# Kernel tuning notes

Measured on AMD Instinct MI355X. Metric: run time of the kernel, lower is better.

Reference implementation:

```python
import jax, jax.numpy as jnp
import numpy as np

N_QUBITS = 16
N_LAYERS = 6
BATCH = 512


def _apply_1q(state, U, q, n, batched):
    """Apply a single-qubit gate U to qubit q of state (B, 2**n).
    U: (2,2) shared, or (B,2,2) per-sample if batched."""
    B = state.shape[0]
    d0, d1 = 2 ** q, 2 ** (n - q - 1)
    s = state.reshape(B, d0, 2, d1)
    if batched:
        s = jnp.einsum('bij,bxjy->bxiy', U, s)
    else:
        s = jnp.einsum('ij,bxjy->bxiy', U, s)
    return s.reshape(B, -1)


def _apply_cnot(state, c, t, n):
    """CNOT with control c, target t on state (B, 2**n)."""
    B = state.shape[0]
    a, b = (c, t) if c < t else (t, c)
    d0, d1, d2 = 2 ** a, 2 ** (b - a - 1), 2 ** (n - b - 1)
    s = state.reshape(B, d0, 2, d1, 2, d2)
    if c < t:  # control = axis 2, target = axis 4: flip target where control==1
        s = jnp.concatenate([s[:, :, :1], jnp.flip(s[:, :, 1:], axis=4)], axis=2)
    else:      # control = axis 4, target = axis 2
        s = jnp.concatenate([s[:, :, :, :, :1], jnp.flip(s[:, :, :, :, 1:], axis=2)], axis=4)
    return s.reshape(B, -1)


def _rx(theta):
    """RX(theta) for a batch of angles -> (B,2,2) complex64."""
    c = jnp.cos(theta * 0.5).astype(jnp.complex64)
    s = (-1j * jnp.sin(theta * 0.5)).astype(jnp.complex64)
    return jnp.stack([jnp.stack([c, s], -1), jnp.stack([s, c], -1)], -2)


def _rot(phi, theta, omega):
    """PennyLane Rot(phi,theta,omega) = RZ(omega) RY(theta) RZ(phi) -> (2,2) complex64."""
    c = jnp.cos(theta * 0.5)
    s = jnp.sin(theta * 0.5)
    m00 = jnp.exp(-0.5j * (phi + omega)) * c
    m01 = -jnp.exp(0.5j * (phi - omega)) * s
    m10 = jnp.exp(-0.5j * (phi - omega)) * s
    m11 = jnp.exp(0.5j * (phi + omega)) * c
    return jnp.stack([jnp.stack([m00, m01]), jnp.stack([m10, m11])]).astype(jnp.complex64)


def _circuit(x, weights, n, n_layers):
    B = x.shape[0]
    state = jnp.zeros((B, 2 ** n), dtype=jnp.complex64).at[:, 0].set(1.0)
    # AngleEmbedding: default rotation is RX(x_q) on wire q (per-sample angles)
    for q in range(n):
        state = _apply_1q(state, _rx(x[:, q]), q, n, batched=True)
    # StronglyEntanglingLayers: Rot on each wire, then ring of CNOTs with range r
    for l in range(n_layers):
        for q in range(n):
            U = _rot(weights[l, q, 0], weights[l, q, 1], weights[l, q, 2])
            state = _apply_1q(state, U, q, n, batched=False)
        r = (l % (n - 1)) + 1  # PennyLane default ranges
        for q in range(n):
            state = _apply_cnot(state, q, (q + r) % n, n)
    # <Z_q> = P(bit_q = 0) - P(bit_q = 1)
    probs = state.real ** 2 + state.imag ** 2  # (B, 2**n)
    exps = []
    for q in range(n):
        p = probs.reshape(B, 2 ** q, 2, -1).sum(axis=(1, 3))  # (B, 2)
        exps.append(p[:, 0] - p[:, 1])
    return jnp.stack(exps, axis=-1)  # (B, n)


def setup_inputs() -> dict:
    key = jax.random.key(0)
    kx, kw = jax.random.split(key)
    x = jax.random.normal(kx, (BATCH, N_QUBITS), dtype=jnp.float32)
    weights = jax.random.normal(kw, (N_LAYERS, N_QUBITS, 3), dtype=jnp.float32)
    return {"x": x, "weights": weights}


def reference(x, weights):
    return _circuit(x, weights, N_QUBITS, N_LAYERS)
```

## Files before the change

### kernel.cpp

```cpp
#include <hip/hip_runtime.h>


#define NTH 512
typedef float v16f __attribute__((ext_vector_type(16)));

template <int I> struct IC { static constexpr int value = I; };
template <int N, int I = 0, typename F>
__device__ __forceinline__ void static_for(F&& f) {
  if constexpr (I < N) { f(IC<I>{}); static_for<N, I + 1>(f); }
}

template <int SH, int E> struct EIdx { static constexpr int v = (E & 1) | ((E >> 1) << SH); };


template <int LB>
__device__ __forceinline__ void rot_local(v16f& ar, v16f& ai, const float* __restrict__ u) {
  const float u00r = u[0], u00i = u[1], u01r = u[2], u01i = u[3];
  const float u10r = u[4], u10i = u[5], u11r = u[6], u11i = u[7];
  static_for<8>([&](auto hc) {
    constexpr int h = hc.value;
    constexpr int e0 = ((h >> LB) << (LB + 1)) | (h & ((1 << LB) - 1));
    constexpr int e1 = e0 | (1 << LB);
    const float axr = ar[e0], axi = ai[e0], bxr = ar[e1], bxi = ai[e1];
    ar[e0] = u00r * axr - u00i * axi + u01r * bxr - u01i * bxi;
    ai[e0] = u00r * axi + u00i * axr + u01r * bxi + u01i * bxr;
    ar[e1] = u10r * axr - u10i * axi + u11r * bxr - u11i * bxi;
    ai[e1] = u10r * axi + u10i * axr + u11r * bxi + u11i * bxr;
  });
}

__device__ __forceinline__ void rot_lane(v16f& ar, v16f& ai, const float* __restrict__ u,
                                         const int m, const int bit) {
  const float car = bit ? u[6] : u[0], cai = bit ? u[7] : u[1];
  const float cbr = bit ? u[4] : u[2], cbi = bit ? u[5] : u[3];
  static_for<16>([&](auto ec) {
    constexpr int e = ec.value;
    const float orr = ar[e], oii = ai[e];
    const float pr = __shfl_xor(orr, m);
    const float pi = __shfl_xor(oii, m);
    ar[e] = car * orr - cai * oii + cbr * pr - cbi * pi;
    ai[e] = car * oii + cai * orr + cbr * pi + cbi * pr;
  });
}

template <int SH, int C>
__device__ __forceinline__ void cnot_lane(v16f& ar, v16f& ai, const int m, const int ibase) {
  if constexpr ((EIdx<SH, 15>::v >> C) & 1) {
    static_for<16>([&](auto ec) {
      constexpr int e = ec.value;
      if constexpr ((EIdx<SH, e>::v >> C) & 1) {
        ar[e] = __shfl_xor(ar[e], m);
        ai[e] = __shfl_xor(ai[e], m);
      }
    });
  } else {
    if ((ibase >> C) & 1) {
      static_for<16>([&](auto ec) {
        constexpr int e = ec.value;
        ar[e] = __shfl_xor(ar[e], m);
        ai[e] = __shfl_xor(ai[e], m);
      });
    }
  }
}

template <int TB, int SH, int C>
__device__ __forceinline__ void cnot_local(v16f& ar, v16f& ai, const int ibase) {
  static_for<8>([&](auto hc) {
    constexpr int h = hc.value;
    constexpr int e0 = ((h >> TB) << (TB + 1)) | (h & ((1 << TB) - 1));
    constexpr int e1 = e0 | (1 << TB);
    if constexpr ((EIdx<SH, 15>::v >> C) & 1) {
      if constexpr ((EIdx<SH, e0>::v >> C) & 1) {
        const float tr = ar[e0], ti = ai[e0];
        ar[e0] = ar[e1]; ai[e0] = ai[e1];
        ar[e1] = tr;     ai[e1] = ti;
      }
    } else {
      const int take = (ibase >> C) & 1;
      const float axr = ar[e0], axi = ai[e0], bxr = ar[e1], bxi = ai[e1];
      ar[e0] = take ? bxr : axr; ai[e0] = take ? bxi : axi;
      ar[e1] = take ? axr : bxr; ai[e1] = take ? axi : bxi;
    }
  });
}

__global__ void qsim_prep(const float* __restrict__ w, float* __restrict__ gm) {
  const int i = threadIdx.x;
  if (i < 96) {
    const float phi = w[i * 3 + 0];
    const float th  = w[i * 3 + 1];
    const float om  = w[i * 3 + 2];
    float st, ct; sincosf(0.5f * th, &st, &ct);
    float sa, ca; sincosf(0.5f * (phi + om), &sa, &ca);
    float sb, cb; sincosf(0.5f * (phi - om), &sb, &cb);
    float* u = gm + i * 8;
    u[0] =  ct * ca; u[1] = -ct * sa;
    u[2] = -st * cb; u[3] = -st * sb;
    u[4] =  st * cb; u[5] = -st * sb;
    u[6] =  ct * ca; u[7] =  ct * sa;
  }
}

template <int L>
__global__ void __launch_bounds__(NTH) sweepP(float2* __restrict__ st,
                                              const float* __restrict__ x,
                                              const float* __restrict__ gm) {
  const int tid = threadIdx.x;
  const int s  = blockIdx.x >> 3;
  const int fb = blockIdx.x & 7;
  const int ibase = (fb << 13) | ((tid & 63) << 4) | ((tid >> 6) << 1);
  const int pbase = (fb << 13) | ((tid & 63) << 1) | ((tid >> 6) << 7);
  float2* __restrict__ base = st + (s << 16) + pbase;
  constexpr int r = L + 1;
  const float* __restrict__ gl = gm + L * 128;
  v16f ar, ai;

  if constexpr (L == 0) {
    __shared__ float iv[16][4];
    if (tid < 16) {
      const float* u = gm + tid * 8;
      float sx, cx; sincosf(0.5f * x[s * 16 + tid], &sx, &cx);
      iv[tid][0] = u[0] * cx + u[3] * sx;
      iv[tid][1] = u[1] * cx - u[2] * sx;
      iv[tid][2] = u[4] * cx + u[7] * sx;
      iv[tid][3] = u[5] * cx - u[6] * sx;
    }
    __syncthreads();
    float Tr = 1.f, Ti = 0.f;
    #pragma unroll
    for (int b = 4; b <= 9; ++b) {
      const int bit = (ibase >> b) & 1;
      const float fr = iv[b][2 * bit], fi = iv[b][2 * bit + 1];
      const float nr = Tr * fr - Ti * fi; Ti = Tr * fi + Ti * fr; Tr = nr;
    }
    #pragma unroll
    for (int b = 13; b <= 15; ++b) {
      const int bit = (ibase >> b) & 1;
      const float fr = iv[b][2 * bit], fi = iv[b][2 * bit + 1];
      const float nr = Tr * fr - Ti * fi; Ti = Tr * fi + Ti * fr; Tr = nr;
    }
    const int b1 = (ibase >> 1) & 1, b2 = (ibase >> 2) & 1, b3 = (ibase >> 3) & 1;
    float Wr[2], Wi[2];
    #pragma unroll
    for (int b0 = 0; b0 < 2; ++b0) {
      const int c1 = b0 ^ b1, c2 = b1 ^ b2, c3 = b2 ^ b3;
      float wr = iv[0][2 * b0], wi = iv[0][2 * b0 + 1];
      { const float fr = iv[1][2 * c1], fi = iv[1][2 * c1 + 1];
        const float nr = wr * fr - wi * fi; wi = wr * fi + wi * fr; wr = nr; }
      { const float fr = iv[2][2 * c2], fi = iv[2][2 * c2 + 1];
        const float nr = wr * fr - wi * fi; wi = wr * fi + wi * fr; wr = nr; }
      { const float fr = iv[3][2 * c3], fi = iv[3][2 * c3 + 1];
        const float nr = wr * fr - wi * fi; wi = wr * fi + wi * fr; wr = nr; }
      Wr[b0] = wr * Tr - wi * Ti; Wi[b0] = wr * Ti + wi * Tr;
    }
    ar[0] = Wr[0]; ai[0] = Wi[0]; ar[1] = Wr[1]; ai[1] = Wi[1];
    static_for<3>([&](auto bc) {
      constexpr int bI = bc.value;
      const int q = 10 + bI;
      const float v0r = iv[q][0], v0i = iv[q][1], v1r = iv[q][2], v1i = iv[q][3];
      static_for<(1 << (bI + 1))>([&](auto kc) {
        constexpr int k = kc.value;
        constexpr int k1 = k | (1 << (bI + 1));
        const float kr = ar[k], ki = ai[k];
        ar[k1] = kr * v1r - ki * v1i; ai[k1] = kr * v1i + ki * v1r;
        ar[k]  = kr * v0r - ki * v0i; ai[k]  = kr * v0i + ki * v0r;
      });
    });
  } else {
    #pragma unroll
    for (int eh = 0; eh < 8; ++eh) {
      const float4 v = *reinterpret_cast<const float4*>(base + (eh << 10));
      ar[2 * eh] = v.x; ai[2 * eh] = v.y; ar[2 * eh + 1] = v.z; ai[2 * eh + 1] = v.w;
    }
    #pragma unroll
    for (int q = 4; q <= 9; ++q)
      rot_lane(ar, ai, gl + q * 8, 1 << (q - 4), (tid >> (q - 4)) & 1);
    rot_local<1>(ar, ai, gl + 80);
    rot_local<2>(ar, ai, gl + 88);
    rot_local<3>(ar, ai, gl + 96);
  }

  constexpr int gstart = (L == 0) ? 3 : (L == 1) ? 2 : (L == 2) ? 1 : 0;
  static_for<(11 - L) - gstart + 1>([&](auto gc) {
    constexpr int g = gstart + gc.value;
    constexpr int t = g + r;
    if constexpr (t <= 9) cnot_lane<10, g>(ar, ai, 1 << (t - 4), ibase);
    else                  cnot_local<t - 9, 10, g>(ar, ai, ibase);
  });

  #pragma unroll
  for (int eh = 0; eh < 8; ++eh)
    *reinterpret_cast<float4*>(base + (eh << 10)) =
        make_float4(ar[2 * eh], ai[2 * eh], ar[2 * eh + 1], ai[2 * eh + 1]);
}

template <int L>
__global__ void __launch_bounds__(NTH) sweepQ(float2* __restrict__ st,
                                              const float* __restrict__ gm,
                                              float* __restrict__ part) {
  const int tid = threadIdx.x;
  const int s  = blockIdx.x >> 3;
  const int fb = blockIdx.x & 7;
  const int ibase = ((tid & 7) << 4) | (((tid >> 3) & 7) << 13) |
                    (((tid >> 6) & 7) << 10) | (fb << 7);
  const int pbase = ((tid & 7) << 1) | (fb << 4) |
                    (((tid >> 6) & 7) << 10) | (((tid >> 3) & 7) << 13);
  float2* __restrict__ base = st + (s << 16) + pbase;
  constexpr int r = L + 1;
  const float* __restrict__ gl = gm + L * 128;
  v16f ar, ai;
  #pragma unroll
  for (int eh = 0; eh < 8; ++eh) {
    const float4 v = *reinterpret_cast<const float4*>(base + (eh << 7));
    ar[2 * eh] = v.x; ai[2 * eh] = v.y; ar[2 * eh + 1] = v.z; ai[2 * eh + 1] = v.w;
  }
  if constexpr (L > 0) {
    rot_lane(ar, ai, gl + 104, 8,  (tid >> 3) & 1);
    rot_lane(ar, ai, gl + 112, 16, (tid >> 4) & 1);
    rot_lane(ar, ai, gl + 120, 32, (tid >> 5) & 1);
  }
  static_for<L + 4>([&](auto gc) {
    constexpr int g = 12 - L + gc.value;
    constexpr int t = (g + r) & 15;
    if constexpr (t >= 13)     cnot_lane<1, g>(ar, ai, 1 << (t - 10), ibase);
    else if constexpr (t >= 4) cnot_lane<1, g>(ar, ai, 1 << (t - 4), ibase);
    else                       cnot_local<t, 1, g>(ar, ai, ibase);
  });

  if constexpr (L < 5) {
    const float* __restrict__ gn = gm + (L + 1) * 128;
    rot_local<0>(ar, ai, gn);
    rot_local<1>(ar, ai, gn + 8);
    rot_local<2>(ar, ai, gn + 16);
    rot_local<3>(ar, ai, gn + 24);
    if constexpr (L == 0) {
      cnot_local<2, 1, 0>(ar, ai, ibase);
      cnot_local<3, 1, 1>(ar, ai, ibase);
    }
    if constexpr (L == 1) {
      cnot_local<3, 1, 0>(ar, ai, ibase);
    }
    #pragma unroll
    for (int eh = 0; eh < 8; ++eh)
      *reinterpret_cast<float4*>(base + (eh << 7)) =
          make_float4(ar[2 * eh], ai[2 * eh], ar[2 * eh + 1], ai[2 * eh + 1]);
  } else {
    __shared__ float red[8][16];
    float tot = 0.f, sl0 = 0.f, sl1 = 0.f, sl2 = 0.f, sl3 = 0.f;
    static_for<16>([&](auto ec) {
      constexpr int e = ec.value;
      const float p = ar[e] * ar[e] + ai[e] * ai[e];
      tot += p;
      if constexpr (e & 1) sl0 -= p; else sl0 += p;
      if constexpr (e & 2) sl1 -= p; else sl1 += p;
      if constexpr (e & 4) sl2 -= p; else sl2 += p;
      if constexpr (e & 8) sl3 -= p; else sl3 += p;
    });
    const float sl[4] = {sl0, sl1, sl2, sl3};
    const int wv = tid >> 6;
    static_for<16>([&](auto qc) {
      constexpr int q = qc.value;
      float v;
      if constexpr (q < 4) v = sl[q];
      else v = ((ibase >> q) & 1) ? -tot : tot;
      v += __shfl_xor(v, 1);  v += __shfl_xor(v, 2);  v += __shfl_xor(v, 4);
      v += __shfl_xor(v, 8);  v += __shfl_xor(v, 16); v += __shfl_xor(v, 32);
      if ((tid & 63) == 0) red[wv][q] = v;
    });
    __syncthreads();
    if (tid < 16) {
      float a = 0.f;
      #pragma unroll
      for (int w8 = 0; w8 < 8; ++w8) a += red[w8][tid];
      part[blockIdx.x * 16 + tid] = a;
    }
  }
}

__global__ void __launch_bounds__(NTH) reduceK(const float* __restrict__ part,
                                               float* __restrict__ out) {
  const int j = blockIdx.x * NTH + threadIdx.x;
  const int s = j >> 4, q = j & 15;
  float a = 0.f;
  #pragma unroll
  for (int fb = 0; fb < 8; ++fb) a += part[(s << 7) + fb * 16 + q];
  out[j] = a;
}

extern "C" void kernel_launch(void* const* d_in, const int* in_sizes, int n_in,
                              void* d_out, int out_size, void* d_ws, size_t ws_size,
                              hipStream_t stream) {
  (void)in_sizes; (void)n_in; (void)out_size;
  const float* x = (const float*)d_in[0];
  const float* w = (const float*)d_in[1];
  float* out = (float*)d_out;
  float* gm   = (float*)d_ws;
  float* part = (float*)((char*)d_ws + 4096);
  float2* st  = (float2*)((char*)d_ws + 524288);

  const size_t avail = ws_size > 524288 ? ws_size - 524288 : 0;
  long long chunk = (long long)(avail / 524288);
  if (chunk > 256) chunk = 256;
  if (chunk < 1) chunk = 1;

  qsim_prep<<<dim3(1), dim3(128), 0, stream>>>(w, gm);
  for (int s0 = 0; s0 < 512; s0 += (int)chunk) {
    const int ns = (512 - s0) < (int)chunk ? (512 - s0) : (int)chunk;
    const dim3 g(ns * 8), b(NTH);
    const float* xs = x + s0 * 16;
    float* pp = part + (size_t)s0 * 128;
    sweepP<0><<<g, b, 0, stream>>>(st, xs, gm);
    sweepQ<0><<<g, b, 0, stream>>>(st, gm, pp);
    sweepP<1><<<g, b, 0, stream>>>(st, xs, gm);
    sweepQ<1><<<g, b, 0, stream>>>(st, gm, pp);
    sweepP<2><<<g, b, 0, stream>>>(st, xs, gm);
    sweepQ<2><<<g, b, 0, stream>>>(st, gm, pp);
    sweepP<3><<<g, b, 0, stream>>>(st, xs, gm);
    sweepQ<3><<<g, b, 0, stream>>>(st, gm, pp);
    sweepP<4><<<g, b, 0, stream>>>(st, xs, gm);
    sweepQ<4><<<g, b, 0, stream>>>(st, gm, pp);
    sweepP<5><<<g, b, 0, stream>>>(st, xs, gm);
    sweepQ<5><<<g, b, 0, stream>>>(st, gm, pp);
  }
  reduceK<<<dim3(16), dim3(NTH), 0, stream>>>(part, out);
}
```

Measured before the change: 1.620 ms.

## Restructure state-vector sweeps with new qubit-to-register mapping and separate final reduction

Changes how qubits map onto register slots, lanes and blocks in both sweep kernels, and moves gates between the P and Q sweeps so the CNOT wrap-around runs at the start of the next P sweep. The final measurement moves into a separate finalK kernel. The aim is to reshape the memory access pattern and gate grouping, for example contiguous float4 loads in sweepP. It adds a thirteenth full pass over the state per chunk, which costs extra global memory traffic.

New measurement: 1.579 ms. -2.5%, faster.

```diff
diff --git a/kernel.cpp b/kernel.cpp
--- a/kernel.cpp
+++ b/kernel.cpp
@@ -109,8 +109,10 @@
   const int tid = threadIdx.x;
   const int s  = blockIdx.x >> 3;
   const int fb = blockIdx.x & 7;
-  const int ibase = (fb << 13) | ((tid & 63) << 4) | ((tid >> 6) << 1);
-  const int pbase = (fb << 13) | ((tid & 63) << 1) | ((tid >> 6) << 7);
+  const int ibase = ((tid & 7) << 4) | (((tid >> 3) & 7) << 7) |
+                    (((tid >> 6) & 7) << 10) | (fb << 13);
+  const int pbase = ((tid & 7) << 1) | (((tid >> 6) & 7) << 7) | (fb << 10) |
+                    (((tid >> 3) & 7) << 13);
   float2* __restrict__ base = st + (s << 16) + pbase;
   constexpr int r = L + 1;
   const float* __restrict__ gl = gm + L * 128;
@@ -129,39 +131,18 @@
     __syncthreads();
     float Tr = 1.f, Ti = 0.f;
     #pragma unroll
-    for (int b = 4; b <= 9; ++b) {
+    for (int b = 4; b <= 15; ++b) {
       const int bit = (ibase >> b) & 1;
       const float fr = iv[b][2 * bit], fi = iv[b][2 * bit + 1];
       const float nr = Tr * fr - Ti * fi; Ti = Tr * fi + Ti * fr; Tr = nr;
     }
-    #pragma unroll
-    for (int b = 13; b <= 15; ++b) {
-      const int bit = (ibase >> b) & 1;
-      const float fr = iv[b][2 * bit], fi = iv[b][2 * bit + 1];
-      const float nr = Tr * fr - Ti * fi; Ti = Tr * fi + Ti * fr; Tr = nr;
-    }
-    const int b1 = (ibase >> 1) & 1, b2 = (ibase >> 2) & 1, b3 = (ibase >> 3) & 1;
-    float Wr[2], Wi[2];
-    #pragma unroll
-    for (int b0 = 0; b0 < 2; ++b0) {
-      const int c1 = b0 ^ b1, c2 = b1 ^ b2, c3 = b2 ^ b3;
-      float wr = iv[0][2 * b0], wi = iv[0][2 * b0 + 1];
-      { const float fr = iv[1][2 * c1], fi = iv[1][2 * c1 + 1];
-        const float nr = wr * fr - wi * fi; wi = wr * fi + wi * fr; wr = nr; }
-      { const float fr = iv[2][2 * c2], fi = iv[2][2 * c2 + 1];
-        const float nr = wr * fr - wi * fi; wi = wr * fi + wi * fr; wr = nr; }
-      { const float fr = iv[3][2 * c3], fi = iv[3][2 * c3 + 1];
-        const float nr = wr * fr - wi * fi; wi = wr * fi + wi * fr; wr = nr; }
-      Wr[b0] = wr * Tr - wi * Ti; Wi[b0] = wr * Ti + wi * Tr;
-    }
-    ar[0] = Wr[0]; ai[0] = Wi[0]; ar[1] = Wr[1]; ai[1] = Wi[1];
-    static_for<3>([&](auto bc) {
+    ar[0] = Tr; ai[0] = Ti;
+    static_for<4>([&](auto bc) {
       constexpr int bI = bc.value;
-      const int q = 10 + bI;
-      const float v0r = iv[q][0], v0i = iv[q][1], v1r = iv[q][2], v1i = iv[q][3];
-      static_for<(1 << (bI + 1))>([&](auto kc) {
+      const float v0r = iv[bI][0], v0i = iv[bI][1], v1r = iv[bI][2], v1i = iv[bI][3];
+      static_for<(1 << bI)>([&](auto kc) {
         constexpr int k = kc.value;
-        constexpr int k1 = k | (1 << (bI + 1));
+        constexpr int k1 = k | (1 << bI);
         const float kr = ar[k], ki = ai[k];
         ar[k1] = kr * v1r - ki * v1i; ai[k1] = kr * v1i + ki * v1r;
         ar[k]  = kr * v0r - ki * v0i; ai[k]  = kr * v0i + ki * v0r;
@@ -170,111 +151,127 @@
   } else {
     #pragma unroll
     for (int eh = 0; eh < 8; ++eh) {
-      const float4 v = *reinterpret_cast<const float4*>(base + (eh << 10));
+      const float4 v = *reinterpret_cast<const float4*>(base + (eh << 4));
       ar[2 * eh] = v.x; ai[2 * eh] = v.y; ar[2 * eh + 1] = v.z; ai[2 * eh + 1] = v.w;
     }
+    static_for<L>([&](auto kc) {
+      constexpr int k = kc.value;
+      constexpr int C = 16 - L + k;
+      if constexpr (k <= 3) cnot_local<k, 1, C>(ar, ai, ibase);
+      else                  cnot_lane<1, C>(ar, ai, 1 << (k - 4), ibase);
+    });
+    rot_local<0>(ar, ai, gl);
+    rot_local<1>(ar, ai, gl + 8);
+    rot_local<2>(ar, ai, gl + 16);
+    rot_local<3>(ar, ai, gl + 24);
     #pragma unroll
     for (int q = 4; q <= 9; ++q)
       rot_lane(ar, ai, gl + q * 8, 1 << (q - 4), (tid >> (q - 4)) & 1);
+  }
+
+  static_for<10 - r>([&](auto gc) {
+    constexpr int g = gc.value;
+    constexpr int t = g + r;
+    if constexpr (t <= 3) cnot_local<t, 1, g>(ar, ai, ibase);
+    else                  cnot_lane<1, g>(ar, ai, 1 << (t - 4), ibase);
+  });
+
+  #pragma unroll
+  for (int eh = 0; eh < 8; ++eh)
+    *reinterpret_cast<float4*>(base + (eh << 4)) =
+        make_float4(ar[2 * eh], ai[2 * eh], ar[2 * eh + 1], ai[2 * eh + 1]);
+}
+
+template <int L>
+__global__ void __launch_bounds__(NTH) sweepQ(float2* __restrict__ st,
+                                              const float* __restrict__ gm) {
+  const int tid = threadIdx.x;
+  const int s  = blockIdx.x >> 3;
+  const int fb = blockIdx.x & 7;
+  const int ibase = ((tid & 7) << 4) | (((tid >> 3) & 7) << 13) |
+                    (((tid >> 6) & 7) << 7) | (fb << 1);
+  const int pbase = ((tid & 7) << 1) | (((tid >> 3) & 7) << 10) |
+                    (((tid >> 6) & 7) << 13) | (fb << 4);
+  float2* __restrict__ base = st + (s << 16) + pbase;
+  constexpr int r = L + 1;
+  const float* __restrict__ gl = gm + L * 128;
+  v16f ar, ai;
+  #pragma unroll
+  for (int eh = 0; eh < 8; ++eh) {
+    const float4 v = *reinterpret_cast<const float4*>(base + (eh << 7));
+    ar[2 * eh] = v.x; ai[2 * eh] = v.y; ar[2 * eh + 1] = v.z; ai[2 * eh + 1] = v.w;
+  }
+  if constexpr (L > 0) {
     rot_local<1>(ar, ai, gl + 80);
     rot_local<2>(ar, ai, gl + 88);
     rot_local<3>(ar, ai, gl + 96);
-  }
-
-  constexpr int gstart = (L == 0) ? 3 : (L == 1) ? 2 : (L == 2) ? 1 : 0;
-  static_for<(11 - L) - gstart + 1>([&](auto gc) {
-    constexpr int g = gstart + gc.value;
+    rot_lane(ar, ai, gl + 104, 8,  (tid >> 3) & 1);
+    rot_lane(ar, ai, gl + 112, 16, (tid >> 4) & 1);
+    rot_lane(ar, ai, gl + 120, 32, (tid >> 5) & 1);
+  }
+  static_for<6>([&](auto gc) {
+    constexpr int g = 10 - r + gc.value;
     constexpr int t = g + r;
-    if constexpr (t <= 9) cnot_lane<10, g>(ar, ai, 1 << (t - 4), ibase);
-    else                  cnot_local<t - 9, 10, g>(ar, ai, ibase);
+    if constexpr (t >= 13) cnot_lane<10, g>(ar, ai, 1 << (t - 10), ibase);
+    else                   cnot_local<t - 9, 10, g>(ar, ai, ibase);
   });
 
   #pragma unroll
   for (int eh = 0; eh < 8; ++eh)
-    *reinterpret_cast<float4*>(base + (eh << 10)) =
+    *reinterpret_cast<float4*>(base + (eh << 7)) =
         make_float4(ar[2 * eh], ai[2 * eh], ar[2 * eh + 1], ai[2 * eh + 1]);
 }
 
-template <int L>
-__global__ void __launch_bounds__(NTH) sweepQ(float2* __restrict__ st,
-                                              const float* __restrict__ gm,
+__global__ void __launch_bounds__(NTH) finalK(const float2* __restrict__ st,
                                               float* __restrict__ part) {
   const int tid = threadIdx.x;
   const int s  = blockIdx.x >> 3;
   const int fb = blockIdx.x & 7;
-  const int ibase = ((tid & 7) << 4) | (((tid >> 3) & 7) << 13) |
-                    (((tid >> 6) & 7) << 10) | (fb << 7);
-  const int pbase = ((tid & 7) << 1) | (fb << 4) |
-                    (((tid >> 6) & 7) << 10) | (((tid >> 3) & 7) << 13);
-  float2* __restrict__ base = st + (s << 16) + pbase;
-  constexpr int r = L + 1;
-  const float* __restrict__ gl = gm + L * 128;
+  const int ibase = ((tid & 7) << 4) | (((tid >> 3) & 7) << 7) |
+                    (((tid >> 6) & 7) << 10) | (fb << 13);
+  const int pbase = ((tid & 7) << 1) | (((tid >> 6) & 7) << 7) | (fb << 10) |
+                    (((tid >> 3) & 7) << 13);
+  const float2* __restrict__ base = st + (s << 16) + pbase;
   v16f ar, ai;
   #pragma unroll
   for (int eh = 0; eh < 8; ++eh) {
-    const float4 v = *reinterpret_cast<const float4*>(base + (eh << 7));
+    const float4 v = *reinterpret_cast<const float4*>(base + (eh << 4));
     ar[2 * eh] = v.x; ai[2 * eh] = v.y; ar[2 * eh + 1] = v.z; ai[2 * eh + 1] = v.w;
   }
-  if constexpr (L > 0) {
-    rot_lane(ar, ai, gl + 104, 8,  (tid >> 3) & 1);
-    rot_lane(ar, ai, gl + 112, 16, (tid >> 4) & 1);
-    rot_lane(ar, ai, gl + 120, 32, (tid >> 5) & 1);
-  }
-  static_for<L + 4>([&](auto gc) {
-    constexpr int g = 12 - L + gc.value;
-    constexpr int t = (g + r) & 15;
-    if constexpr (t >= 13)     cnot_lane<1, g>(ar, ai, 1 << (t - 10), ibase);
-    else if constexpr (t >= 4) cnot_lane<1, g>(ar, ai, 1 << (t - 4), ibase);
-    else                       cnot_local<t, 1, g>(ar, ai, ibase);
-  });
-
-  if constexpr (L < 5) {
-    const float* __restrict__ gn = gm + (L + 1) * 128;
-    rot_local<0>(ar, ai, gn);
-    rot_local<1>(ar, ai, gn + 8);
-    rot_local<2>(ar, ai, gn + 16);
-    rot_local<3>(ar, ai, gn + 24);
-    if constexpr (L == 0) {
-      cnot_local<2, 1, 0>(ar, ai, ibase);
-      cnot_local<3, 1, 1>(ar, ai, ibase);
-    }
-    if constexpr (L == 1) {
-      cnot_local<3, 1, 0>(ar, ai, ibase);
-    }
+  static_for<6>([&](auto kc) {
+    constexpr int k = kc.value;
+    constexpr int C = 10 + k;
+    if constexpr (k <= 3) cnot_local<k, 1, C>(ar, ai, ibase);
+    else                  cnot_lane<1, C>(ar, ai, 1 << (k - 4), ibase);
+  });
+  __shared__ float red[8][16];
+  float tot = 0.f, sl0 = 0.f, sl1 = 0.f, sl2 = 0.f, sl3 = 0.f;
+  static_for<16>([&](auto ec) {
+    constexpr int e = ec.value;
+    const float p = ar[e] * ar[e] + ai[e] * ai[e];
+    tot += p;
+    if constexpr (e & 1) sl0 -= p; else sl0 += p;
+    if constexpr (e & 2) sl1 -= p; else sl1 += p;
+    if constexpr (e & 4) sl2 -= p; else sl2 += p;
+    if constexpr (e & 8) sl3 -= p; else sl3 += p;
+  });
+  const float sl[4] = {sl0, sl1, sl2, sl3};
+  const int wv = tid >> 6;
+  static_for<16>([&](auto qc) {
+    constexpr int q = qc.value;
+    float v;
+    if constexpr (q < 4) v = sl[q];
+    else v = ((ibase >> q) & 1) ? -tot : tot;
+    v += __shfl_xor(v, 1);  v += __shfl_xor(v, 2);  v += __shfl_xor(v, 4);
+    v += __shfl_xor(v, 8);  v += __shfl_xor(v, 16); v += __shfl_xor(v, 32);
+    if ((tid & 63) == 0) red[wv][q] = v;
+  });
+  __syncthreads();
+  if (tid < 16) {
+    float a = 0.f;
     #pragma unroll
-    for (int eh = 0; eh < 8; ++eh)
-      *reinterpret_cast<float4*>(base + (eh << 7)) =
-          make_float4(ar[2 * eh], ai[2 * eh], ar[2 * eh + 1], ai[2 * eh + 1]);
-  } else {
-    __shared__ float red[8][16];
-    float tot = 0.f, sl0 = 0.f, sl1 = 0.f, sl2 = 0.f, sl3 = 0.f;
-    static_for<16>([&](auto ec) {
-      constexpr int e = ec.value;
-      const float p = ar[e] * ar[e] + ai[e] * ai[e];
-      tot += p;
-      if constexpr (e & 1) sl0 -= p; else sl0 += p;
-      if constexpr (e & 2) sl1 -= p; else sl1 += p;
-      if constexpr (e & 4) sl2 -= p; else sl2 += p;
-      if constexpr (e & 8) sl3 -= p; else sl3 += p;
-    });
-    const float sl[4] = {sl0, sl1, sl2, sl3};
-    const int wv = tid >> 6;
-    static_for<16>([&](auto qc) {
-      constexpr int q = qc.value;
-      float v;
-      if constexpr (q < 4) v = sl[q];
-      else v = ((ibase >> q) & 1) ? -tot : tot;
-      v += __shfl_xor(v, 1);  v += __shfl_xor(v, 2);  v += __shfl_xor(v, 4);
-      v += __shfl_xor(v, 8);  v += __shfl_xor(v, 16); v += __shfl_xor(v, 32);
-      if ((tid & 63) == 0) red[wv][q] = v;
-    });
-    __syncthreads();
-    if (tid < 16) {
-      float a = 0.f;
-      #pragma unroll
-      for (int w8 = 0; w8 < 8; ++w8) a += red[w8][tid];
-      part[blockIdx.x * 16 + tid] = a;
-    }
+    for (int w8 = 0; w8 < 8; ++w8) a += red[w8][tid];
+    part[blockIdx.x * 16 + tid] = a;
   }
 }
 
@@ -311,17 +308,18 @@
     const float* xs = x + s0 * 16;
     float* pp = part + (size_t)s0 * 128;
     sweepP<0><<<g, b, 0, stream>>>(st, xs, gm);
-    sweepQ<0><<<g, b, 0, stream>>>(st, gm, pp);
+    sweepQ<0><<<g, b, 0, stream>>>(st, gm);
     sweepP<1><<<g, b, 0, stream>>>(st, xs, gm);
-    sweepQ<1><<<g, b, 0, stream>>>(st, gm, pp);
+    sweepQ<1><<<g, b, 0, stream>>>(st, gm);
     sweepP<2><<<g, b, 0, stream>>>(st, xs, gm);
-    sweepQ<2><<<g, b, 0, stream>>>(st, gm, pp);
+    sweepQ<2><<<g, b, 0, stream>>>(st, gm);
     sweepP<3><<<g, b, 0, stream>>>(st, xs, gm);
-    sweepQ<3><<<g, b, 0, stream>>>(st, gm, pp);
+    sweepQ<3><<<g, b, 0, stream>>>(st, gm);
     sweepP<4><<<g, b, 0, stream>>>(st, xs, gm);
-    sweepQ<4><<<g, b, 0, stream>>>(st, gm, pp);
+    sweepQ<4><<<g, b, 0, stream>>>(st, gm);
     sweepP<5><<<g, b, 0, stream>>>(st, xs, gm);
-    sweepQ<5><<<g, b, 0, stream>>>(st, gm, pp);
+    sweepQ<5><<<g, b, 0, stream>>>(st, gm);
+    finalK<<<g, b, 0, stream>>>(st, pp);
   }
   reduceK<<<dim3(16), dim3(NTH), 0, stream>>>(part, out);
 }
```
